# Performance work log

Measured on AMD Instinct MI355X. Metric: run time of the kernel, lower is better.

Reference implementation:

```python
import math
import jax, jax.numpy as jnp
import numpy as np

HIDDEN = 4096
N_HEADS = 32
HEAD_DIM = HIDDEN // N_HEADS  # 128
N_GROUPS = 4                  # n_heads_in_group
N_KV_HEADS = N_HEADS // N_GROUPS  # 8
ROPE_THETA = 500000.0


def setup_inputs() -> dict:
    key = jax.random.key(0)
    ks = jax.random.split(key, 6)
    B, S = 2, 2048
    hidden_states = jax.random.normal(ks[0], (B, S, HIDDEN), dtype=jnp.float32)
    position_ids = jnp.broadcast_to(jnp.arange(S, dtype=jnp.int64), (B, S))
    sc = 1.0 / math.sqrt(HIDDEN)
    # weights stored as [in, out] (x @ W == torch Linear with weight W.T)
    wq = jax.random.normal(ks[1], (HIDDEN, N_HEADS * HEAD_DIM), dtype=jnp.float32) * sc
    wk = jax.random.normal(ks[2], (HIDDEN, N_KV_HEADS * HEAD_DIM), dtype=jnp.float32) * sc
    wv = jax.random.normal(ks[3], (HIDDEN, N_KV_HEADS * HEAD_DIM), dtype=jnp.float32) * sc
    wo = jax.random.normal(ks[4], (HIDDEN, HIDDEN), dtype=jnp.float32) * sc
    return {"hidden_states": hidden_states, "position_ids": position_ids,
            "wq": wq, "wk": wk, "wv": wv, "wo": wo}


def _rotate_half(x):
    x1, x2 = jnp.split(x, 2, axis=-1)
    return jnp.concatenate((-x2, x1), axis=-1)


def _rope_cos_sin(position_ids, dtype):
    inv_freq = 1.0 / (ROPE_THETA ** (jnp.arange(0, HEAD_DIM, 2, dtype=jnp.float32) / HEAD_DIM))
    freqs = position_ids.astype(jnp.float32)[:, :, None] * inv_freq[None, None, :]  # [B,S,hd/2]
    emb = jnp.concatenate((freqs, freqs), axis=-1)  # [B,S,hd]
    return jnp.cos(emb).astype(dtype), jnp.sin(emb).astype(dtype)


def reference(hidden_states, position_ids, wq, wk, wv, wo):
    B, S, _ = hidden_states.shape
    dt = hidden_states.dtype
    q = (hidden_states @ wq).reshape(B, S, N_HEADS, HEAD_DIM).transpose(0, 2, 1, 3)      # [B,H,S,hd]
    k = (hidden_states @ wk).reshape(B, S, N_KV_HEADS, HEAD_DIM).transpose(0, 2, 1, 3)   # [B,KV,S,hd]
    v = (hidden_states @ wv).reshape(B, S, N_KV_HEADS, HEAD_DIM).transpose(0, 2, 1, 3)
    cos, sin = _rope_cos_sin(position_ids, dt)
    cos, sin = cos[:, None], sin[:, None]  # unsqueeze head dim
    q = q * cos + _rotate_half(q) * sin
    k = k * cos + _rotate_half(k) * sin
    # GQA repeat_kv
    k = jnp.repeat(k, N_GROUPS, axis=1)  # [B,H,S,hd]
    v = jnp.repeat(v, N_GROUPS, axis=1)
    scores = jnp.einsum('bhqd,bhkd->bhqk', q, k) / math.sqrt(HEAD_DIM)
    causal = jnp.tril(jnp.ones((S, S), dtype=bool))
    scores = jnp.where(causal[None, None], scores, jnp.float32(-jnp.inf).astype(dt))
    attn = jax.nn.softmax(scores.astype(jnp.float32), axis=-1).astype(dt)
    out = jnp.einsum('bhqk,bhkd->bhqd', attn, v)          # [B,H,S,hd]
    out = out.transpose(0, 2, 1, 3).reshape(B, S, HIDDEN)  # [B,S,hidden]
    return out @ wo
```

## Files before the change

kernel.cpp:

```cpp
#include <hip/hip_runtime.h>

typedef unsigned short u16;
typedef float f32x4 __attribute__((ext_vector_type(4)));
typedef short bf16x8 __attribute__((ext_vector_type(8)));
typedef u16 u16x8 __attribute__((ext_vector_type(8)));

#define HID 4096
#define SEQ 2048
#define LDQKV 6144

__device__ __forceinline__ u16 f2b(float f) {
    union { float f; unsigned u; } v; v.f = f;
    unsigned r = v.u + 0x7FFFu + ((v.u >> 16) & 1u);
    return (u16)(r >> 16);
}
__device__ __forceinline__ float b2f(u16 u) {
    union { unsigned u; float f; } v; v.u = ((unsigned)u) << 16;
    return v.f;
}
__device__ __forceinline__ f32x4 mfma16(bf16x8 a, bf16x8 b, f32x4 c) {
    return __builtin_amdgcn_mfma_f32_16x16x32_bf16(a, b, c, 0, 0, 0);
}
__device__ __forceinline__ void gload16(const void* g, void* l) {
    __builtin_amdgcn_global_load_lds(
        (const __attribute__((address_space(1))) unsigned int*)g,
        (__attribute__((address_space(3))) unsigned int*)l,
        16, 0, 0);
}

__global__ void k_cvt_bf16(const float* __restrict__ x, u16* __restrict__ y) {
    int i = blockIdx.x * 256 + threadIdx.x;
    const f32x4* p = (const f32x4*)(x + (size_t)i * 8);
    f32x4 a = p[0], b = p[1];
    u16x8 o;
    o[0]=f2b(a.x); o[1]=f2b(a.y); o[2]=f2b(a.z); o[3]=f2b(a.w);
    o[4]=f2b(b.x); o[5]=f2b(b.y); o[6]=f2b(b.z); o[7]=f2b(b.w);
    *(u16x8*)(y + (size_t)i * 8) = o;
}

__global__ void k_twc(const float* __restrict__ W, int N, u16* __restrict__ WT) {
    __shared__ float tile[64][68];
    int t = threadIdx.x;
    int n0 = blockIdx.x * 64, k0 = blockIdx.y * 64;
#pragma unroll
    for (int i = 0; i < 4; i++) {
        int idx = i * 256 + t;
        int r = idx >> 4;
        int c = (idx & 15) * 4;
        f32x4 v = *(const f32x4*)(W + (size_t)(k0 + r) * N + n0 + c);
        tile[r][c] = v.x; tile[r][c+1] = v.y; tile[r][c+2] = v.z; tile[r][c+3] = v.w;
    }
    __syncthreads();
    int n_l = t >> 2;
    int c0 = (t & 3) * 16;
    u16x8 o0, o1;
#pragma unroll
    for (int u = 0; u < 8; u++) {
        o0[u] = f2b(tile[c0 + u][n_l]);
        o1[u] = f2b(tile[c0 + 8 + u][n_l]);
    }
    u16* dst = WT + (size_t)(n0 + n_l) * 4096 + k0 + c0;
    *(u16x8*)dst = o0;
    *(u16x8*)(dst + 8) = o1;
}

__global__ void k_rope_tab(float* __restrict__ ct, float* __restrict__ st) {
    int idx = blockIdx.x * 256 + threadIdx.x;
    int row = idx >> 6, i = idx & 63;
    float p = (float)(row & (SEQ - 1));
    float inv = exp2f(-(float)i * 0.29582835f);
    float f = p * inv;
    ct[idx] = cosf(f);
    st[idx] = sinf(f);
}

__global__ void k_rope(u16* __restrict__ qkv, const float* __restrict__ ct, const float* __restrict__ st) {
    int t = threadIdx.x, w = t >> 6, lane = t & 63;
    int hr = blockIdx.x * 4 + w;
    int row = hr / 40, hh = hr % 40;
    int col0 = (hh < 32) ? hh * 128 : 4096 + (hh - 32) * 128;
    u16* p = qkv + (size_t)row * LDQKV + col0;
    float c = ct[row * 64 + lane], s = st[row * 64 + lane];
    float x1 = b2f(p[lane]), x2 = b2f(p[lane + 64]);
    p[lane]      = f2b(x1 * c - x2 * s);
    p[lane + 64] = f2b(x2 * c + x1 * s);
}

template <int MODE>
__global__ __launch_bounds__(256) void k_gemm(const u16* __restrict__ A, const u16* __restrict__ Bt,
                                              void* __restrict__ C, u16* __restrict__ Vt,
                                              int K, int ldc) {
    __shared__ __align__(16) u16 Al[128 * 64];
    __shared__ __align__(16) u16 Bl[128 * 64];
    int t = threadIdx.x, w = t >> 6, lane = t & 63;
    int lr = lane & 15, lg = lane >> 4;
    int wr = w >> 1, wc = w & 1;
    int by = blockIdx.y, bx = blockIdx.x;

    const char* gA[4]; const char* gB[4];
    char* lA[4]; char* lB[4];
#pragma unroll
    for (int i = 0; i < 4; i++) {
        int o = i * 4096 + w * 1024 + lane * 16;
        int r = o >> 7, cb = o & 127;
        int scb = cb ^ ((r & 7) << 4);
        gA[i] = (const char*)A + (size_t)(by * 128 + r) * K * 2 + scb;
        gB[i] = (const char*)Bt + (size_t)(bx * 128 + r) * K * 2 + scb;
        lA[i] = (char*)Al + i * 4096 + w * 1024;
        lB[i] = (char*)Bl + i * 4096 + w * 1024;
    }

    f32x4 acc[4][4] = {};
    int nk = K >> 6;
    for (int kt = 0; kt < nk; kt++) {
#pragma unroll
        for (int i = 0; i < 4; i++) gload16(gA[i], lA[i]);
#pragma unroll
        for (int i = 0; i < 4; i++) gload16(gB[i], lB[i]);
#pragma unroll
        for (int i = 0; i < 4; i++) { gA[i] += 128; gB[i] += 128; }
        __syncthreads();
#pragma unroll
        for (int kk = 0; kk < 2; kk++) {
            bf16x8 af[4], bfr[4];
#pragma unroll
            for (int m = 0; m < 4; m++) {
                int row = wr * 64 + m * 16 + lr;
                af[m] = *(const bf16x8*)((const char*)Al + row * 128 + ((kk * 64 + lg * 16) ^ ((row & 7) << 4)));
            }
#pragma unroll
            for (int n = 0; n < 4; n++) {
                int row = wc * 64 + n * 16 + lr;
                bfr[n] = *(const bf16x8*)((const char*)Bl + row * 128 + ((kk * 64 + lg * 16) ^ ((row & 7) << 4)));
            }
#pragma unroll
            for (int m = 0; m < 4; m++)
#pragma unroll
                for (int n = 0; n < 4; n++)
                    acc[m][n] = mfma16(af[m], bfr[n], acc[m][n]);
        }
        __syncthreads();
    }

    int rowBase = by * 128 + wr * 64;
    int colBase = bx * 128 + wc * 64;
    if (MODE == 0) {
        bool isV = (colBase >= 5120);
        if (!isV) {
            u16* Cb = (u16*)C;
#pragma unroll
            for (int m = 0; m < 4; m++)
#pragma unroll
                for (int n = 0; n < 4; n++)
#pragma unroll
                    for (int j = 0; j < 4; j++) {
                        int grow = rowBase + m * 16 + lg * 4 + j;
                        int gcol = colBase + n * 16 + lr;
                        Cb[(size_t)grow * ldc + gcol] = f2b(acc[m][n][j]);
                    }
        } else {
#pragma unroll
            for (int m = 0; m < 4; m++)
#pragma unroll
                for (int n = 0; n < 4; n++)
#pragma unroll
                    for (int j = 0; j < 4; j++) {
                        int grow = rowBase + m * 16 + lg * 4 + j;
                        int gcol = colBase + n * 16 + lr;
                        int cv = gcol - 5120;
                        int kvh = cv >> 7, d = cv & 127;
                        int b = grow >> 11, s2 = grow & 2047;
                        Vt[(size_t)((b * 8 + kvh) * 128 + d) * 2048 + s2] = f2b(acc[m][n][j]);
                    }
        }
    } else {
        float* Cf = (float*)C;
#pragma unroll
        for (int m = 0; m < 4; m++)
#pragma unroll
            for (int n = 0; n < 4; n++)
#pragma unroll
                for (int j = 0; j < 4; j++) {
                    int grow = rowBase + m * 16 + lg * 4 + j;
                    int gcol = colBase + n * 16 + lr;
                    Cf[(size_t)grow * ldc + gcol] = acc[m][n][j];
                }
    }
}

__global__ __launch_bounds__(256) void k_attn(const u16* __restrict__ qkv, const u16* __restrict__ Vt,
                                              u16* __restrict__ out) {
    __shared__ __align__(16) u16 Kl[64 * 128];
    __shared__ __align__(16) u16 Vl[128 * 64];
    __shared__ __align__(16) u16 Pl[4 * 16 * 72];
    int t = threadIdx.x, w = t >> 6, lane = t & 63;
    int lr = lane & 15, lg = lane >> 4;
    int qt = blockIdx.x, h = blockIdx.y, b = blockIdx.z;
    int kvh = h >> 2;
    int q0 = qt * 64;

    bf16x8 qf[4];
    {
        int qrow = q0 + w * 16 + lr;
        const u16* qp = qkv + (size_t)(b * SEQ + qrow) * LDQKV + h * 128 + lg * 8;
#pragma unroll
        for (int kd = 0; kd < 4; kd++) qf[kd] = *(const bf16x8*)(qp + kd * 32);
    }

    f32x4 acc[8] = {};
    float m_r[4], l_r[4];
#pragma unroll
    for (int j = 0; j < 4; j++) { m_r[j] = -INFINITY; l_r[j] = 0.f; }
    const float scale = 0.08838834764831845f;

    const char* Kbase = (const char*)qkv + (size_t)b * SEQ * (LDQKV * 2) + (size_t)(4096 + kvh * 128) * 2;
    const char* Vbase = (const char*)Vt + (size_t)(b * 8 + kvh) * 128 * 4096;
    u16* Pw = Pl + w * 16 * 72;

    for (int kv = 0; kv <= qt; kv++) {
        int kv0 = kv * 64;
#pragma unroll
        for (int i = 0; i < 4; i++) {
            int o = i * 4096 + w * 1024 + lane * 16;
            {
                int sk = o >> 8, cb = o & 255;
                int scb = cb ^ ((sk & 7) << 4);
                gload16(Kbase + (size_t)(kv0 + sk) * (LDQKV * 2) + scb, (char*)Kl + i * 4096 + w * 1024);
            }
            {
                int d = o >> 7, cb = o & 127;
                int scb = cb ^ ((d & 7) << 4);
                gload16(Vbase + (size_t)d * 4096 + kv0 * 2 + scb, (char*)Vl + i * 4096 + w * 1024);
            }
        }
        __syncthreads();

        f32x4 sf[4];
#pragma unroll
        for (int f = 0; f < 4; f++) {
            f32x4 s = {};
            int skr = f * 16 + lr;
            const char* kr = (const char*)Kl + skr * 256;
            int sw = (skr & 7) << 4;
#pragma unroll
            for (int kd = 0; kd < 4; kd++) {
                bf16x8 kb = *(const bf16x8*)(kr + ((kd * 64 + lg * 16) ^ sw));
                s = mfma16(qf[kd], kb, s);
            }
            sf[f] = s;
        }

        int qrow_g = q0 + w * 16 + lg * 4;
        float mnew[4], alpha[4];
#pragma unroll
        for (int j = 0; j < 4; j++) {
            float mx = -INFINITY;
#pragma unroll
            for (int f = 0; f < 4; f++) {
                float v = sf[f][j] * scale;
                int colg = kv0 + f * 16 + lr;
                if (colg > qrow_g + j) v = -INFINITY;
                sf[f][j] = v;
                mx = fmaxf(mx, v);
            }
#pragma unroll
            for (int d = 1; d < 16; d <<= 1) mx = fmaxf(mx, __shfl_xor(mx, d));
            mnew[j] = fmaxf(m_r[j], mx);
            alpha[j] = __expf(m_r[j] - mnew[j]);
            m_r[j] = mnew[j];
        }
#pragma unroll
        for (int j = 0; j < 4; j++) {
            float sum = 0.f;
#pragma unroll
            for (int f = 0; f < 4; f++) {
                float p = __expf(sf[f][j] - mnew[j]);
                sf[f][j] = p;
                sum += p;
            }
#pragma unroll
            for (int d = 1; d < 16; d <<= 1) sum += __shfl_xor(sum, d);
            l_r[j] = l_r[j] * alpha[j] + sum;
        }
#pragma unroll
        for (int nf = 0; nf < 8; nf++)
#pragma unroll
            for (int j = 0; j < 4; j++) acc[nf][j] *= alpha[j];

#pragma unroll
        for (int f = 0; f < 4; f++)
#pragma unroll
            for (int j = 0; j < 4; j++)
                Pw[(lg * 4 + j) * 72 + f * 16 + lr] = f2b(sf[f][j]);

        bf16x8 pa[2];
#pragma unroll
        for (int kk = 0; kk < 2; kk++)
            pa[kk] = *(const bf16x8*)(Pw + lr * 72 + kk * 32 + lg * 8);
#pragma unroll
        for (int nf = 0; nf < 8; nf++) {
            int d = nf * 16 + lr;
            const char* vr = (const char*)Vl + d * 128;
            int swv = (d & 7) << 4;
#pragma unroll
            for (int kk = 0; kk < 2; kk++) {
                bf16x8 vb = *(const bf16x8*)(vr + ((kk * 64 + lg * 16) ^ swv));
                acc[nf] = mfma16(pa[kk], vb, acc[nf]);
            }
        }
        __syncthreads();
    }

#pragma unroll
    for (int nf = 0; nf < 8; nf++)
#pragma unroll
        for (int j = 0; j < 4; j++) {
            float v = acc[nf][j] / l_r[j];
            int qrow = q0 + w * 16 + lg * 4 + j;
            out[(size_t)(b * SEQ + qrow) * 4096 + h * 128 + nf * 16 + lr] = f2b(v);
        }
}

extern "C" void kernel_launch(void* const* d_in, const int* in_sizes, int n_in,
                              void* d_out, int out_size, void* d_ws, size_t ws_size,
                              hipStream_t stream) {
    const float* hs  = (const float*)d_in[0];
    const float* wq  = (const float*)d_in[2];
    const float* wk  = (const float*)d_in[3];
    const float* wv  = (const float*)d_in[4];
    const float* wo  = (const float*)d_in[5];
    float* out = (float*)d_out;
    char* ws = (char*)d_ws;

    u16* Xb   = (u16*)(ws);
    u16* Wt   = (u16*)(ws + 33554432);
    u16* WoT  = (u16*)(ws + 83886080);
    u16* QKV  = (u16*)(ws + 117440512);
    u16* Vt   = (u16*)(ws + 167772160);
    float* ct = (float*)(ws + 176160768);
    float* st = (float*)(ws + 177209344);
    u16* AO   = Xb;

    k_cvt_bf16<<<8192, 256, 0, stream>>>(hs, Xb);
    k_twc<<<dim3(64, 64), 256, 0, stream>>>(wq, 4096, Wt);
    k_twc<<<dim3(16, 64), 256, 0, stream>>>(wk, 1024, Wt + (size_t)4096 * 4096);
    k_twc<<<dim3(16, 64), 256, 0, stream>>>(wv, 1024, Wt + (size_t)5120 * 4096);
    k_twc<<<dim3(64, 64), 256, 0, stream>>>(wo, 4096, WoT);
    k_rope_tab<<<1024, 256, 0, stream>>>(ct, st);
    k_gemm<0><<<dim3(48, 32), 256, 0, stream>>>(Xb, Wt, QKV, Vt, 4096, LDQKV);
    k_rope<<<40960, 256, 0, stream>>>(QKV, ct, st);
    k_attn<<<dim3(32, 32, 2), 256, 0, stream>>>(QKV, Vt, AO);
    k_gemm<1><<<dim3(32, 32), 256, 0, stream>>>(AO, WoT, out, nullptr, 4096, 4096);
}
```

Before: 954.4 us.

## Share GQA K/V tiles across heads in attention and balance causal work

Each attention block now covers one KV head, with each of its four waves handling a different query head of the group. The shared K/V tile is therefore loaded once per group rather than once per head. Each block processes a pair of 32-row query tiles (p and 63-p), which evens out the causal workload across blocks, and K loads are double-buffered so the next tile is prefetched during compute. The costs are a grid four times smaller (512 blocks), more registers for two row-fragments per wave, and extra shared memory for the second K buffer.

```diff
diff --git a/kernel.cpp b/kernel.cpp
--- a/kernel.cpp
+++ b/kernel.cpp
@@ -190,135 +190,168 @@
 
 __global__ __launch_bounds__(256) void k_attn(const u16* __restrict__ qkv, const u16* __restrict__ Vt,
                                               u16* __restrict__ out) {
-    __shared__ __align__(16) u16 Kl[64 * 128];
+    __shared__ __align__(16) u16 Kl[2][64 * 128];
     __shared__ __align__(16) u16 Vl[128 * 64];
-    __shared__ __align__(16) u16 Pl[4 * 16 * 72];
+    __shared__ __align__(16) u16 Pl[4][32 * 72];
     int t = threadIdx.x, w = t >> 6, lane = t & 63;
     int lr = lane & 15, lg = lane >> 4;
-    int qt = blockIdx.x, h = blockIdx.y, b = blockIdx.z;
-    int kvh = h >> 2;
-    int q0 = qt * 64;
-
-    bf16x8 qf[4];
-    {
-        int qrow = q0 + w * 16 + lr;
-        const u16* qp = qkv + (size_t)(b * SEQ + qrow) * LDQKV + h * 128 + lg * 8;
-#pragma unroll
-        for (int kd = 0; kd < 4; kd++) qf[kd] = *(const bf16x8*)(qp + kd * 32);
-    }
-
-    f32x4 acc[8] = {};
-    float m_r[4], l_r[4];
-#pragma unroll
-    for (int j = 0; j < 4; j++) { m_r[j] = -INFINITY; l_r[j] = 0.f; }
+    int p = blockIdx.x;
+    int kvh = blockIdx.y;
+    int b = blockIdx.z;
+    int h = kvh * 4 + w;
     const float scale = 0.08838834764831845f;
 
     const char* Kbase = (const char*)qkv + (size_t)b * SEQ * (LDQKV * 2) + (size_t)(4096 + kvh * 128) * 2;
     const char* Vbase = (const char*)Vt + (size_t)(b * 8 + kvh) * 128 * 4096;
-    u16* Pw = Pl + w * 16 * 72;
-
-    for (int kv = 0; kv <= qt; kv++) {
-        int kv0 = kv * 64;
+    u16* Pw = Pl[w];
+
+#pragma unroll 1
+    for (int half = 0; half < 2; half++) {
+        int qa = half ? (63 - p) : p;
+        int q0 = qa * 32;
+        int nt = qa / 2 + 1;
+
+        bf16x8 qf[2][4];
+#pragma unroll
+        for (int m = 0; m < 2; m++)
+#pragma unroll
+            for (int kd = 0; kd < 4; kd++)
+                qf[m][kd] = *(const bf16x8*)(qkv + (size_t)(b * SEQ + q0 + m * 16 + lr) * LDQKV
+                                                  + h * 128 + kd * 32 + lg * 8);
+
+        f32x4 acc[2][8] = {};
+        float m_r[2][4], l_r[2][4];
+#pragma unroll
+        for (int m = 0; m < 2; m++)
+#pragma unroll
+            for (int j = 0; j < 4; j++) { m_r[m][j] = -INFINITY; l_r[m][j] = 0.f; }
+
 #pragma unroll
         for (int i = 0; i < 4; i++) {
             int o = i * 4096 + w * 1024 + lane * 16;
-            {
-                int sk = o >> 8, cb = o & 255;
-                int scb = cb ^ ((sk & 7) << 4);
-                gload16(Kbase + (size_t)(kv0 + sk) * (LDQKV * 2) + scb, (char*)Kl + i * 4096 + w * 1024);
-            }
-            {
+            int sk = o >> 8, cb = o & 255;
+            int scb = cb ^ ((sk & 7) << 4);
+            gload16(Kbase + (size_t)sk * (LDQKV * 2) + scb, (char*)Kl[0] + i * 4096 + w * 1024);
+        }
+        __syncthreads();
+
+        int cur = 0;
+#pragma unroll 1
+        for (int kv = 0; kv < nt; kv++) {
+            int kv0 = kv * 64;
+#pragma unroll
+            for (int i = 0; i < 4; i++) {
+                int o = i * 4096 + w * 1024 + lane * 16;
                 int d = o >> 7, cb = o & 127;
                 int scb = cb ^ ((d & 7) << 4);
-                gload16(Vbase + (size_t)d * 4096 + kv0 * 2 + scb, (char*)Vl + i * 4096 + w * 1024);
-            }
+                gload16(Vbase + (size_t)d * 4096 + (size_t)kv0 * 2 + scb, (char*)Vl + i * 4096 + w * 1024);
+            }
+            if (kv + 1 < nt) {
+#pragma unroll
+                for (int i = 0; i < 4; i++) {
+                    int o = i * 4096 + w * 1024 + lane * 16;
+                    int sk = o >> 8, cb = o & 255;
+                    int scb = cb ^ ((sk & 7) << 4);
+                    gload16(Kbase + (size_t)(kv0 + 64 + sk) * (LDQKV * 2) + scb,
+                            (char*)Kl[cur ^ 1] + i * 4096 + w * 1024);
+                }
+            }
+
+            f32x4 sf[2][4] = {};
+            const char* Kc = (const char*)Kl[cur];
+#pragma unroll
+            for (int f = 0; f < 4; f++) {
+                int skr = f * 16 + lr;
+                const char* kr = Kc + skr * 256;
+                int sw = (skr & 7) << 4;
+#pragma unroll
+                for (int kd = 0; kd < 4; kd++) {
+                    bf16x8 kb = *(const bf16x8*)(kr + ((kd * 64 + lg * 16) ^ sw));
+#pragma unroll
+                    for (int m = 0; m < 2; m++) sf[m][f] = mfma16(qf[m][kd], kb, sf[m][f]);
+                }
+            }
+
+#pragma unroll
+            for (int m = 0; m < 2; m++) {
+                int qrow_g = q0 + m * 16 + lg * 4;
+                float mnew[4], alpha[4];
+#pragma unroll
+                for (int j = 0; j < 4; j++) {
+                    float mx = -INFINITY;
+#pragma unroll
+                    for (int f = 0; f < 4; f++) {
+                        float v = sf[m][f][j] * scale;
+                        int colg = kv0 + f * 16 + lr;
+                        if (colg > qrow_g + j) v = -INFINITY;
+                        sf[m][f][j] = v;
+                        mx = fmaxf(mx, v);
+                    }
+#pragma unroll
+                    for (int d = 1; d < 16; d <<= 1) mx = fmaxf(mx, __shfl_xor(mx, d));
+                    mnew[j] = fmaxf(m_r[m][j], mx);
+                    alpha[j] = __expf(m_r[m][j] - mnew[j]);
+                    m_r[m][j] = mnew[j];
+                }
+#pragma unroll
+                for (int j = 0; j < 4; j++) {
+                    float sum = 0.f;
+#pragma unroll
+                    for (int f = 0; f < 4; f++) {
+                        float pv = __expf(sf[m][f][j] - mnew[j]);
+                        sf[m][f][j] = pv;
+                        sum += pv;
+                    }
+#pragma unroll
+                    for (int d = 1; d < 16; d <<= 1) sum += __shfl_xor(sum, d);
+                    l_r[m][j] = l_r[m][j] * alpha[j] + sum;
+                }
+#pragma unroll
+                for (int nf = 0; nf < 8; nf++)
+#pragma unroll
+                    for (int j = 0; j < 4; j++) acc[m][nf][j] *= alpha[j];
+#pragma unroll
+                for (int f = 0; f < 4; f++)
+#pragma unroll
+                    for (int j = 0; j < 4; j++)
+                        Pw[(m * 16 + lg * 4 + j) * 72 + f * 16 + lr] = f2b(sf[m][f][j]);
+            }
+
+            __syncthreads();
+
+            bf16x8 pa[2][2];
+#pragma unroll
+            for (int m = 0; m < 2; m++)
+#pragma unroll
+                for (int kk = 0; kk < 2; kk++)
+                    pa[m][kk] = *(const bf16x8*)(Pw + (m * 16 + lr) * 72 + kk * 32 + lg * 8);
+#pragma unroll
+            for (int nf = 0; nf < 8; nf++) {
+                int d = nf * 16 + lr;
+                const char* vr = (const char*)Vl + d * 128;
+                int swv = (d & 7) << 4;
+#pragma unroll
+                for (int kk = 0; kk < 2; kk++) {
+                    bf16x8 vb = *(const bf16x8*)(vr + ((kk * 64 + lg * 16) ^ swv));
+#pragma unroll
+                    for (int m = 0; m < 2; m++) acc[m][nf] = mfma16(pa[m][kk], vb, acc[m][nf]);
+                }
+            }
+            __syncthreads();
+            cur ^= 1;
         }
-        __syncthreads();
-
-        f32x4 sf[4];
-#pragma unroll
-        for (int f = 0; f < 4; f++) {
-            f32x4 s = {};
-            int skr = f * 16 + lr;
-            const char* kr = (const char*)Kl + skr * 256;
-            int sw = (skr & 7) << 4;
-#pragma unroll
-            for (int kd = 0; kd < 4; kd++) {
-                bf16x8 kb = *(const bf16x8*)(kr + ((kd * 64 + lg * 16) ^ sw));
-                s = mfma16(qf[kd], kb, s);
-            }
-            sf[f] = s;
-        }
-
-        int qrow_g = q0 + w * 16 + lg * 4;
-        float mnew[4], alpha[4];
-#pragma unroll
-        for (int j = 0; j < 4; j++) {
-            float mx = -INFINITY;
-#pragma unroll
-            for (int f = 0; f < 4; f++) {
-                float v = sf[f][j] * scale;
-                int colg = kv0 + f * 16 + lr;
-                if (colg > qrow_g + j) v = -INFINITY;
-                sf[f][j] = v;
-                mx = fmaxf(mx, v);
-            }
-#pragma unroll
-            for (int d = 1; d < 16; d <<= 1) mx = fmaxf(mx, __shfl_xor(mx, d));
-            mnew[j] = fmaxf(m_r[j], mx);
-            alpha[j] = __expf(m_r[j] - mnew[j]);
-            m_r[j] = mnew[j];
-        }
-#pragma unroll
-        for (int j = 0; j < 4; j++) {
-            float sum = 0.f;
-#pragma unroll
-            for (int f = 0; f < 4; f++) {
-                float p = __expf(sf[f][j] - mnew[j]);
-                sf[f][j] = p;
-                sum += p;
-            }
-#pragma unroll
-            for (int d = 1; d < 16; d <<= 1) sum += __shfl_xor(sum, d);
-            l_r[j] = l_r[j] * alpha[j] + sum;
-        }
-#pragma unroll
-        for (int nf = 0; nf < 8; nf++)
-#pragma unroll
-            for (int j = 0; j < 4; j++) acc[nf][j] *= alpha[j];
-
-#pragma unroll
-        for (int f = 0; f < 4; f++)
-#pragma unroll
-            for (int j = 0; j < 4; j++)
-                Pw[(lg * 4 + j) * 72 + f * 16 + lr] = f2b(sf[f][j]);
-
-        bf16x8 pa[2];
-#pragma unroll
-        for (int kk = 0; kk < 2; kk++)
-            pa[kk] = *(const bf16x8*)(Pw + lr * 72 + kk * 32 + lg * 8);
-#pragma unroll
-        for (int nf = 0; nf < 8; nf++) {
-            int d = nf * 16 + lr;
-            const char* vr = (const char*)Vl + d * 128;
-            int swv = (d & 7) << 4;
-#pragma unroll
-            for (int kk = 0; kk < 2; kk++) {
-                bf16x8 vb = *(const bf16x8*)(vr + ((kk * 64 + lg * 16) ^ swv));
-                acc[nf] = mfma16(pa[kk], vb, acc[nf]);
-            }
-        }
-        __syncthreads();
-    }
-
-#pragma unroll
-    for (int nf = 0; nf < 8; nf++)
-#pragma unroll
-        for (int j = 0; j < 4; j++) {
-            float v = acc[nf][j] / l_r[j];
-            int qrow = q0 + w * 16 + lg * 4 + j;
-            out[(size_t)(b * SEQ + qrow) * 4096 + h * 128 + nf * 16 + lr] = f2b(v);
-        }
+
+#pragma unroll
+        for (int m = 0; m < 2; m++)
+#pragma unroll
+            for (int nf = 0; nf < 8; nf++)
+#pragma unroll
+                for (int j = 0; j < 4; j++) {
+                    int qrow = q0 + m * 16 + lg * 4 + j;
+                    out[(size_t)(b * SEQ + qrow) * 4096 + h * 128 + nf * 16 + lr]
+                        = f2b(acc[m][nf][j] / l_r[m][j]);
+                }
+    }
 }
 
 extern "C" void kernel_launch(void* const* d_in, const int* in_sizes, int n_in,
@@ -349,6 +382,6 @@
     k_rope_tab<<<1024, 256, 0, stream>>>(ct, st);
     k_gemm<0><<<dim3(48, 32), 256, 0, stream>>>(Xb, Wt, QKV, Vt, 4096, LDQKV);
     k_rope<<<40960, 256, 0, stream>>>(QKV, ct, st);
-    k_attn<<<dim3(32, 32, 2), 256, 0, stream>>>(QKV, Vt, AO);
+    k_attn<<<dim3(32, 8, 2), 256, 0, stream>>>(QKV, Vt, AO);
     k_gemm<1><<<dim3(32, 32), 256, 0, stream>>>(AO, WoT, out, nullptr, 4096, 4096);
 }
```

New measurement: 856.3 us. -10.3%, faster.
